# Optimization experiments

Measured on AMD Instinct MI355X. Metric: run time of the kernel, lower is better.

The kernel has to match this reference:

```python
import jax, jax.numpy as jnp
import numpy as np
import math

H = 8
C = 512
HIDE = 2048
LN_EPS = 1e-6


def setup_inputs() -> dict:
    key = jax.random.key(0)
    ks = jax.random.split(key, 9)
    B, N = 4, 2048
    std = 0.02
    return {
        "q": jax.random.normal(ks[0], (B, N, C), jnp.float32),
        "k": jax.random.normal(ks[1], (B, N, C), jnp.float32),
        "v": jax.random.normal(ks[2], (B, N, C), jnp.float32),
        "fc1_w": jax.random.normal(ks[3], (HIDE, C), jnp.float32) * std,
        "fc1_b": jnp.zeros((HIDE,), jnp.float32),
        "fc2_w": jax.random.normal(ks[4], (C, HIDE), jnp.float32) * std,
        "fc2_b": jnp.zeros((C,), jnp.float32),
        "ln1_w": jnp.ones((C,), jnp.float32),
        "ln1_b": jnp.zeros((C,), jnp.float32),
        "ln2_w": jnp.ones((C,), jnp.float32),
        "ln2_b": jnp.zeros((C,), jnp.float32),
    }


def _layernorm(x, w, b):
    mu = jnp.mean(x, axis=-1, keepdims=True)
    var = jnp.var(x, axis=-1, keepdims=True)
    return (x - mu) * jax.lax.rsqrt(var + LN_EPS) * w + b


def _mha(q, k, v):
    B, N, _ = q.shape
    hd = C // H
    # [B, H, N, hd]
    qh = q.reshape(B, N, H, hd).transpose(0, 2, 1, 3)
    kh = k.reshape(B, N, H, hd).transpose(0, 2, 1, 3)
    vh = v.reshape(B, N, H, hd).transpose(0, 2, 1, 3)
    scores = jnp.einsum('bhqd,bhkd->bhqk', qh, kh) / math.sqrt(hd)
    probs = jax.nn.softmax(scores, axis=-1)
    out = jnp.einsum('bhqk,bhkd->bhqd', probs, vh)
    return out.transpose(0, 2, 1, 3).reshape(B, N, C)


def reference(q, k, v, fc1_w, fc1_b, fc2_w, fc2_b, ln1_w, ln1_b, ln2_w, ln2_b):
    attn = _mha(q, k, v)
    q2 = _layernorm(q + attn, ln1_w, ln1_b)
    h = jax.nn.gelu(q2 @ fc1_w.T + fc1_b, approximate=False)
    mlp = h @ fc2_w.T + fc2_b
    return _layernorm(q2 + mlp, ln2_w, ln2_b)
```

## Files before the change

kernel.cpp:

```cpp
#include <hip/hip_runtime.h>
#include <math.h>

typedef unsigned short u16;
typedef __bf16 bf16_t;
typedef bf16_t bf16x4 __attribute__((ext_vector_type(4)));
typedef bf16_t bf16x8 __attribute__((ext_vector_type(8)));
typedef short s16x4 __attribute__((ext_vector_type(4)));
typedef float f32x4 __attribute__((ext_vector_type(4)));

typedef const __attribute__((address_space(1))) void* gcp;
typedef __attribute__((address_space(3))) void* lcp;

#define BB 4
#define NN 2048
#define CC 512
#define HH 8
#define HD 64
#define HIDE_ 2048
#define TT (BB*NN)

#if __has_builtin(__builtin_amdgcn_exp2f)
#define EXP2(x) __builtin_amdgcn_exp2f(x)
#else
#define EXP2(x) __expf((x) * 0.69314718055994531f)
#endif

#if __has_builtin(__builtin_amdgcn_rcpf)
#define RCP(x) __builtin_amdgcn_rcpf(x)
#else
#define RCP(x) (1.0f / (x))
#endif

__device__ __forceinline__ u16 f2bf(float f) {
  unsigned u = __float_as_uint(f);
  u += 0x7FFF + ((u >> 16) & 1);
  return (u16)(u >> 16);
}

__device__ __forceinline__ void bf8_to_f(const u16* p, float* f) {
  uint4 u = *(const uint4*)p;
  f[0] = __uint_as_float(u.x << 16); f[1] = __uint_as_float(u.x & 0xffff0000u);
  f[2] = __uint_as_float(u.y << 16); f[3] = __uint_as_float(u.y & 0xffff0000u);
  f[4] = __uint_as_float(u.z << 16); f[5] = __uint_as_float(u.z & 0xffff0000u);
  f[6] = __uint_as_float(u.w << 16); f[7] = __uint_as_float(u.w & 0xffff0000u);
}

__device__ __forceinline__ float gelu_tanh(float x) {
  float y = 0.7978845608028654f * x * (1.0f + 0.044715f * x * x);
  float a = y * 2.8853900817779268f;
  a = fminf(fmaxf(a, -30.0f), 30.0f);
  float e = EXP2(a);
  float t = (e - 1.0f) * RCP(e + 1.0f);
  return 0.5f * x * (1.0f + t);
}

__global__ __launch_bounds__(256) void prep_kernel(const float* __restrict__ q,
                                                   const float* __restrict__ k,
                                                   const float* __restrict__ fc1w,
                                                   const float* __restrict__ fc2w,
                                                   const float* __restrict__ v,
                                                   u16* __restrict__ qb,
                                                   u16* __restrict__ kb,
                                                   u16* __restrict__ w1b,
                                                   u16* __restrict__ w2b,
                                                   u16* __restrict__ vtb,
                                                   float qscale) {
  __shared__ __align__(16) u16 T[64 * 72];
  int bid = blockIdx.x, tid = threadIdx.x;
  if (bid < 5120) {
    const float* in;
    u16* out;
    int rel;
    float sc = 1.0f;
    if (bid < 2048)      { in = q;    out = qb;  rel = bid;        sc = qscale; }
    else if (bid < 4096) { in = k;    out = kb;  rel = bid - 2048; }
    else if (bid < 4608) { in = fc1w; out = w1b; rel = bid - 4096; }
    else                 { in = fc2w; out = w2b; rel = bid - 4608; }
    int i = (rel * 256 + tid) * 8;
    float4 a = *(const float4*)(in + i);
    float4 b2 = *(const float4*)(in + i + 4);
    u16 r[8] = {f2bf(a.x * sc), f2bf(a.y * sc), f2bf(a.z * sc), f2bf(a.w * sc),
                f2bf(b2.x * sc), f2bf(b2.y * sc), f2bf(b2.z * sc), f2bf(b2.w * sc)};
    *(uint4*)(out + i) = *(const uint4*)r;
    return;
  }
  int tv = bid - 5120;
  int j0 = (tv & 31) * 64;
  int bh = tv >> 5;
  int b = bh >> 3, h = bh & 7;
#pragma unroll
  for (int i = 0; i < 16; i++) {
    int idx = i * 256 + tid;
    int j = idx >> 6, d = idx & 63;
    T[d * 72 + j] = f2bf(v[((size_t)(b * NN + j0 + j)) * CC + h * 64 + d]);
  }
  __syncthreads();
#pragma unroll
  for (int i = 0; i < 16; i++) {
    int idx = i * 256 + tid;
    int d = idx >> 6, j = idx & 63;
    vtb[((size_t)(bh * 64 + d)) * NN + j0 + j] = T[d * 72 + j];
  }
}

__global__ __launch_bounds__(256, 4) void attn_kernel(const u16* __restrict__ qb,
                                                      const u16* __restrict__ kb,
                                                      const u16* __restrict__ vtb,
                                                      u16* __restrict__ ou,
                                                      float* __restrict__ lsum) {
  __shared__ __align__(16) u16 Ks[64 * 64];
  __shared__ __align__(16) u16 Vs[64 * 64];
  int tid = threadIdx.x, wave = tid >> 6, lane = tid & 63;
  int l15 = lane & 15, quad = lane >> 4;
  int r7 = l15 & 7;
  int bid = blockIdx.x;
  int half = blockIdx.y;
  int qt = bid & 15, h = (bid >> 4) & 7, b = bid >> 7;
  int qw = qt * 128 + wave * 32;
  int j0base = half * 1024;

  u16* ou_ = ou + (size_t)half * TT * CC;
  float* ls_ = lsum + (size_t)half * TT * HH;

  size_t qbase = ((size_t)(b * NN + qw + l15)) * CC + h * 64 + quad * 8;
  bf16x8 qfA0 = *(const bf16x8*)&qb[qbase];
  bf16x8 qfA1 = *(const bf16x8*)&qb[qbase + 32];
  bf16x8 qfB0 = *(const bf16x8*)&qb[qbase + (size_t)16 * CC];
  bf16x8 qfB1 = *(const bf16x8*)&qb[qbase + (size_t)16 * CC + 32];

  int rl = lane >> 3;
  int cb = (lane & 7) ^ rl;
  int rK = wave * 16 + rl;
  size_t vtbase = ((size_t)(b * HH + h)) * 64 * NN;
  const u16* kp0 = kb + ((size_t)(b * NN + j0base + rK)) * CC + h * 64 + cb * 8;
  const u16* kp1 = kp0 + (size_t)8 * CC;
  const u16* vp0 = vtb + vtbase + (size_t)rK * NN + j0base + cb * 8;
  const u16* vp1 = vp0 + (size_t)8 * NN;
  lcp lK0 = (lcp)&Ks[wave * 16 * 64];
  lcp lK1 = (lcp)&Ks[wave * 16 * 64 + 8 * 64];
  lcp lV0 = (lcp)&Vs[wave * 16 * 64];
  lcp lV1 = (lcp)&Vs[wave * 16 * 64 + 8 * 64];

  float lA = 0.f, lB = 0.f;
  f32x4 oA[4] = {}, oB[4] = {};

  for (int kt = 0; kt < 16; kt++) {
    __syncthreads();
    __builtin_amdgcn_global_load_lds((gcp)kp0, lK0, 16, 0, 0);
    __builtin_amdgcn_global_load_lds((gcp)kp1, lK1, 16, 0, 0);
    __builtin_amdgcn_global_load_lds((gcp)vp0, lV0, 16, 0, 0);
    __builtin_amdgcn_global_load_lds((gcp)vp1, lV1, 16, 0, 0);
    kp0 += (size_t)64 * CC; kp1 += (size_t)64 * CC;
    vp0 += 64; vp1 += 64;
    __syncthreads();

    s16x4 pfA[4], pfB[4];
#pragma unroll
    for (int nt = 0; nt < 4; nt++) {
      const u16* krow = &Ks[(nt * 16 + l15) * 64];
      bf16x8 k0 = *(const bf16x8*)&krow[(quad ^ r7) * 8];
      bf16x8 k1 = *(const bf16x8*)&krow[((quad + 4) ^ r7) * 8];
      f32x4 zA = {0.f, 0.f, 0.f, 0.f}, zB = {0.f, 0.f, 0.f, 0.f};
      zA = __builtin_amdgcn_mfma_f32_16x16x32_bf16(k0, qfA0, zA, 0, 0, 0);
      zA = __builtin_amdgcn_mfma_f32_16x16x32_bf16(k1, qfA1, zA, 0, 0, 0);
      zB = __builtin_amdgcn_mfma_f32_16x16x32_bf16(k0, qfB0, zB, 0, 0, 0);
      zB = __builtin_amdgcn_mfma_f32_16x16x32_bf16(k1, qfB1, zB, 0, 0, 0);
      float a0 = EXP2(zA[0]), a1 = EXP2(zA[1]), a2 = EXP2(zA[2]), a3 = EXP2(zA[3]);
      float b0 = EXP2(zB[0]), b1 = EXP2(zB[1]), b2 = EXP2(zB[2]), b3 = EXP2(zB[3]);
      lA += (a0 + a1) + (a2 + a3);
      lB += (b0 + b1) + (b2 + b3);
      bf16x4 ta = {(bf16_t)a0, (bf16_t)a1, (bf16_t)a2, (bf16_t)a3};
      bf16x4 tb = {(bf16_t)b0, (bf16_t)b1, (bf16_t)b2, (bf16_t)b3};
      pfA[nt] = __builtin_bit_cast(s16x4, ta);
      pfB[nt] = __builtin_bit_cast(s16x4, tb);
    }
#pragma unroll
    for (int dt = 0; dt < 4; dt++) {
      const u16* vrow = &Vs[(dt * 16 + l15) * 64];
#pragma unroll
      for (int nt = 0; nt < 4; nt++) {
        s16x4 vf = *(const s16x4*)
            &vrow[((nt * 2 + (quad >> 1)) ^ r7) * 8 + (quad & 1) * 4];
        oA[dt] = __builtin_amdgcn_mfma_f32_16x16x16bf16_1k(vf, pfA[nt], oA[dt], 0, 0, 0);
        oB[dt] = __builtin_amdgcn_mfma_f32_16x16x16bf16_1k(vf, pfB[nt], oB[dt], 0, 0, 0);
      }
    }
  }

  lA += __shfl_xor(lA, 16, 64);
  lA += __shfl_xor(lA, 32, 64);
  lB += __shfl_xor(lB, 16, 64);
  lB += __shfl_xor(lB, 32, 64);
  if (quad == 0) {
    ls_[(size_t)(b * NN + qw + l15) * HH + h] = lA;
    ls_[(size_t)(b * NN + qw + 16 + l15) * HH + h] = lB;
  }
  size_t obase = ((size_t)(b * NN + qw + l15)) * CC + h * 64 + quad * 4;
#pragma unroll
  for (int dt = 0; dt < 4; dt++) {
    u16 ra[4] = {f2bf(oA[dt][0]), f2bf(oA[dt][1]), f2bf(oA[dt][2]), f2bf(oA[dt][3])};
    u16 rb[4] = {f2bf(oB[dt][0]), f2bf(oB[dt][1]), f2bf(oB[dt][2]), f2bf(oB[dt][3])};
    *(uint2*)&ou_[obase + dt * 16] = *(const uint2*)ra;
    *(uint2*)&ou_[obase + (size_t)16 * CC + dt * 16] = *(const uint2*)rb;
  }
}

__global__ __launch_bounds__(256) void ln1_kernel(const u16* __restrict__ qb,
                                                  const u16* __restrict__ ou,
                                                  const float* __restrict__ lsum,
                                                  const float* __restrict__ w,
                                                  const float* __restrict__ bb,
                                                  u16* __restrict__ outb,
                                                  float inv_qs) {
  int tid = threadIdx.x;
  int row = blockIdx.x * 4 + (tid >> 6);
  int lane = tid & 63;
  int h = lane >> 3;
  size_t base = (size_t)row * CC + lane * 8;
  const u16* ou1 = ou + (size_t)TT * CC;
  const float* ls1 = lsum + (size_t)TT * HH;
  float li = lsum[(size_t)row * HH + h] + ls1[(size_t)row * HH + h];
  float inv = 1.0f / li;
  float a[8], c[8], d[8];
  bf8_to_f(qb + base, a);
  bf8_to_f(ou + base, c);
  bf8_to_f(ou1 + base, d);
  float x[8];
#pragma unroll
  for (int i = 0; i < 8; i++) x[i] = a[i] * inv_qs + (c[i] + d[i]) * inv;
  float sum = 0.f, sq = 0.f;
#pragma unroll
  for (int i = 0; i < 8; i++) { sum += x[i]; sq += x[i] * x[i]; }
#pragma unroll
  for (int msk = 1; msk < 64; msk <<= 1) {
    sum += __shfl_xor(sum, msk, 64);
    sq += __shfl_xor(sq, msk, 64);
  }
  float mu = sum * (1.0f / CC);
  float var = sq * (1.0f / CC) - mu * mu;
  float rs = rsqrtf(var + 1e-6f);
  int col = lane * 8;
  float4 w0 = *(const float4*)(w + col);
  float4 w1 = *(const float4*)(w + col + 4);
  float4 b0 = *(const float4*)(bb + col);
  float4 b1 = *(const float4*)(bb + col + 4);
  float wv[8] = {w0.x, w0.y, w0.z, w0.w, w1.x, w1.y, w1.z, w1.w};
  float bv[8] = {b0.x, b0.y, b0.z, b0.w, b1.x, b1.y, b1.z, b1.w};
  u16 r[8];
#pragma unroll
  for (int i = 0; i < 8; i++) r[i] = f2bf((x[i] - mu) * rs * wv[i] + bv[i]);
  *(uint4*)(outb + base) = *(const uint4*)r;
}

__global__ __launch_bounds__(256) void ln2_kernel(const u16* __restrict__ q2b,
                                                  const u16* __restrict__ mp,
                                                  const float* __restrict__ fb,
                                                  const float* __restrict__ w,
                                                  const float* __restrict__ bb,
                                                  float* __restrict__ outf) {
  int tid = threadIdx.x;
  int row = blockIdx.x * 4 + (tid >> 6);
  int lane = tid & 63;
  size_t base = (size_t)row * CC + lane * 8;
  const u16* mp1 = mp + (size_t)TT * CC;
  int col = lane * 8;
  float a[8], c[8], d[8];
  bf8_to_f(q2b + base, a);
  bf8_to_f(mp + base, c);
  bf8_to_f(mp1 + base, d);
  float4 f0 = *(const float4*)(fb + col);
  float4 f1 = *(const float4*)(fb + col + 4);
  float fbv[8] = {f0.x, f0.y, f0.z, f0.w, f1.x, f1.y, f1.z, f1.w};
  float x[8];
#pragma unroll
  for (int i = 0; i < 8; i++) x[i] = a[i] + c[i] + d[i] + fbv[i];
  float sum = 0.f, sq = 0.f;
#pragma unroll
  for (int i = 0; i < 8; i++) { sum += x[i]; sq += x[i] * x[i]; }
#pragma unroll
  for (int msk = 1; msk < 64; msk <<= 1) {
    sum += __shfl_xor(sum, msk, 64);
    sq += __shfl_xor(sq, msk, 64);
  }
  float mu = sum * (1.0f / CC);
  float var = sq * (1.0f / CC) - mu * mu;
  float rs = rsqrtf(var + 1e-6f);
  float4 w0 = *(const float4*)(w + col);
  float4 w1 = *(const float4*)(w + col + 4);
  float4 b0 = *(const float4*)(bb + col);
  float4 b1 = *(const float4*)(bb + col + 4);
  float wv[8] = {w0.x, w0.y, w0.z, w0.w, w1.x, w1.y, w1.z, w1.w};
  float bv[8] = {b0.x, b0.y, b0.z, b0.w, b1.x, b1.y, b1.z, b1.w};
  float y[8];
#pragma unroll
  for (int i = 0; i < 8; i++) y[i] = (x[i] - mu) * rs * wv[i] + bv[i];
  *(float4*)(outf + base) = make_float4(y[0], y[1], y[2], y[3]);
  *(float4*)(outf + base + 4) = make_float4(y[4], y[5], y[6], y[7]);
}

__global__ __launch_bounds__(256) void gemm_fc1(const u16* __restrict__ A,
                                                const u16* __restrict__ Bw,
                                                const float* __restrict__ bias,
                                                u16* __restrict__ outb,
                                                int M, int Nn, int K) {
  __shared__ __align__(16) u16 As[128 * 32];
  __shared__ __align__(16) u16 Bs[128 * 32];
  int tid = threadIdx.x, wave = tid >> 6, lane = tid & 63;
  int l15 = lane & 15, quad = lane >> 4;
  int m0 = blockIdx.y * 128, n0 = blockIdx.x * 128;
  int wm = (wave >> 1) * 64, wn = (wave & 1) * 64;
  int w32 = wave * 32;
  int lrow = lane >> 2, lcol = (lane & 3) * 8;
  const u16* Ap = &A[(size_t)(m0 + w32 + lrow) * K + lcol];
  const u16* Bp = &Bw[(size_t)(n0 + w32 + lrow) * K + lcol];
  const u16* Ap2 = Ap + (size_t)16 * K;
  const u16* Bp2 = Bp + (size_t)16 * K;
  lcp lAs0 = (lcp)&As[w32 * 32];
  lcp lAs1 = (lcp)&As[(w32 + 16) * 32];
  lcp lBs0 = (lcp)&Bs[w32 * 32];
  lcp lBs1 = (lcp)&Bs[(w32 + 16) * 32];
  f32x4 acc[4][4] = {};

  for (int kk = 0; kk < K; kk += 32) {
    __syncthreads();
    __builtin_amdgcn_global_load_lds((gcp)(Ap + kk), lAs0, 16, 0, 0);
    __builtin_amdgcn_global_load_lds((gcp)(Ap2 + kk), lAs1, 16, 0, 0);
    __builtin_amdgcn_global_load_lds((gcp)(Bp + kk), lBs0, 16, 0, 0);
    __builtin_amdgcn_global_load_lds((gcp)(Bp2 + kk), lBs1, 16, 0, 0);
    __syncthreads();
    bf16x8 af[4], bf[4];
#pragma unroll
    for (int am = 0; am < 4; am++)
      af[am] = *(const bf16x8*)&As[(wm + am * 16 + l15) * 32 + quad * 8];
#pragma unroll
    for (int bn = 0; bn < 4; bn++)
      bf[bn] = *(const bf16x8*)&Bs[(wn + bn * 16 + l15) * 32 + quad * 8];
#pragma unroll
    for (int am = 0; am < 4; am++)
#pragma unroll
      for (int bn = 0; bn < 4; bn++)
        acc[am][bn] =
            __builtin_amdgcn_mfma_f32_16x16x32_bf16(af[am], bf[bn], acc[am][bn], 0, 0, 0);
  }

#pragma unroll
  for (int am = 0; am < 4; am++)
#pragma unroll
    for (int bn = 0; bn < 4; bn++) {
      int rowi = m0 + wm + am * 16 + quad * 4;
      int col = n0 + wn + bn * 16 + l15;
      float bcol = bias[col];
#pragma unroll
      for (int r = 0; r < 4; r++) {
        float val = gelu_tanh(acc[am][bn][r] + bcol);
        outb[(size_t)(rowi + r) * Nn + col] = f2bf(val);
      }
    }
}

__global__ __launch_bounds__(256) void gemm_fc2_sk(const u16* __restrict__ A,
                                                   const u16* __restrict__ Bw,
                                                   u16* __restrict__ outb,
                                                   int M, int Nn, int K, int Ksplit) {
  __shared__ __align__(16) u16 As[128 * 32];
  __shared__ __align__(16) u16 Bs[128 * 32];
  int tid = threadIdx.x, wave = tid >> 6, lane = tid & 63;
  int l15 = lane & 15, quad = lane >> 4;
  int m0 = blockIdx.y * 128, n0 = blockIdx.x * 128;
  int kbeg = blockIdx.z * Ksplit;
  u16* outz = outb + (size_t)blockIdx.z * TT * CC;
  int wm = (wave >> 1) * 64, wn = (wave & 1) * 64;
  int w32 = wave * 32;
  int lrow = lane >> 2, lcol = (lane & 3) * 8;
  const u16* Ap = &A[(size_t)(m0 + w32 + lrow) * K + lcol];
  const u16* Bp = &Bw[(size_t)(n0 + w32 + lrow) * K + lcol];
  const u16* Ap2 = Ap + (size_t)16 * K;
  const u16* Bp2 = Bp + (size_t)16 * K;
  lcp lAs0 = (lcp)&As[w32 * 32];
  lcp lAs1 = (lcp)&As[(w32 + 16) * 32];
  lcp lBs0 = (lcp)&Bs[w32 * 32];
  lcp lBs1 = (lcp)&Bs[(w32 + 16) * 32];
  f32x4 acc[4][4] = {};

  for (int kk = kbeg; kk < kbeg + Ksplit; kk += 32) {
    __syncthreads();
    __builtin_amdgcn_global_load_lds((gcp)(Ap + kk), lAs0, 16, 0, 0);
    __builtin_amdgcn_global_load_lds((gcp)(Ap2 + kk), lAs1, 16, 0, 0);
    __builtin_amdgcn_global_load_lds((gcp)(Bp + kk), lBs0, 16, 0, 0);
    __builtin_amdgcn_global_load_lds((gcp)(Bp2 + kk), lBs1, 16, 0, 0);
    __syncthreads();
    bf16x8 af[4], bf[4];
#pragma unroll
    for (int am = 0; am < 4; am++)
      af[am] = *(const bf16x8*)&As[(wm + am * 16 + l15) * 32 + quad * 8];
#pragma unroll
    for (int bn = 0; bn < 4; bn++)
      bf[bn] = *(const bf16x8*)&Bs[(wn + bn * 16 + l15) * 32 + quad * 8];
#pragma unroll
    for (int am = 0; am < 4; am++)
#pragma unroll
      for (int bn = 0; bn < 4; bn++)
        acc[am][bn] =
            __builtin_amdgcn_mfma_f32_16x16x32_bf16(af[am], bf[bn], acc[am][bn], 0, 0, 0);
  }

#pragma unroll
  for (int am = 0; am < 4; am++)
#pragma unroll
    for (int bn = 0; bn < 4; bn++) {
      int rowi = m0 + wm + am * 16 + quad * 4;
      int col = n0 + wn + bn * 16 + l15;
#pragma unroll
      for (int r = 0; r < 4; r++)
        outz[(size_t)(rowi + r) * Nn + col] = f2bf(acc[am][bn][r]);
    }
}

extern "C" void kernel_launch(void* const* d_in, const int* in_sizes, int n_in,
                              void* d_out, int out_size, void* d_ws, size_t ws_size,
                              hipStream_t stream) {
  const float* q = (const float*)d_in[0];
  const float* k = (const float*)d_in[1];
  const float* v = (const float*)d_in[2];
  const float* fc1_w = (const float*)d_in[3];
  const float* fc1_b = (const float*)d_in[4];
  const float* fc2_w = (const float*)d_in[5];
  const float* fc2_b = (const float*)d_in[6];
  const float* ln1_w = (const float*)d_in[7];
  const float* ln1_b = (const float*)d_in[8];
  const float* ln2_w = (const float*)d_in[9];
  const float* ln2_b = (const float*)d_in[10];
  float* out = (float*)d_out;

  char* ws = (char*)d_ws;
  size_t off = 0;
  u16* qb = (u16*)(ws + off); off += (size_t)TT * CC * 2;
  u16* kb = (u16*)(ws + off); off += (size_t)TT * CC * 2;
  u16* vtb = (u16*)(ws + off); off += (size_t)TT * CC * 2;
  u16* w1b = (u16*)(ws + off); off += (size_t)HIDE_ * CC * 2;
  u16* w2b = (u16*)(ws + off); off += (size_t)CC * HIDE_ * 2;
  u16* ou = (u16*)(ws + off); off += (size_t)2 * TT * CC * 2;
  float* lsum = (float*)(ws + off); off += (size_t)2 * TT * HH * 4;
  u16* q2b = (u16*)(ws + off); off += (size_t)TT * CC * 2;
  u16* hbuf = (u16*)(ws + off); off += (size_t)TT * HIDE_ * 2;
  u16* mp = (u16*)(ws + off); off += (size_t)2 * TT * CC * 2;

  const float QS = 0.18033688011112042f;
  const float INV_QS = 5.5451774444795623f;
  prep_kernel<<<6144, 256, 0, stream>>>(q, k, fc1_w, fc2_w, v, qb, kb, w1b, w2b, vtb, QS);
  attn_kernel<<<dim3(512, 2), 256, 0, stream>>>(qb, kb, vtb, ou, lsum);
  ln1_kernel<<<2048, 256, 0, stream>>>(qb, ou, lsum, ln1_w, ln1_b, q2b, INV_QS);
  gemm_fc1<<<dim3(16, 64), 256, 0, stream>>>(q2b, w1b, fc1_b, hbuf, TT, HIDE_, CC);
  gemm_fc2_sk<<<dim3(4, 64, 2), 256, 0, stream>>>(hbuf, w2b, mp, TT, CC, HIDE_, 1024);
  ln2_kernel<<<2048, 256, 0, stream>>>(q2b, mp, fc2_b, ln2_w, ln2_b, out);
}
```

Measured before the change: 242.3 us.

## Drop bf16 q copy and deepen GEMM K-tiles to 64 with swizzled LDS

```diff
diff --git a/kernel.cpp b/kernel.cpp
--- a/kernel.cpp
+++ b/kernel.cpp
@@ -45,6 +45,14 @@
   f[6] = __uint_as_float(u.w << 16); f[7] = __uint_as_float(u.w & 0xffff0000u);
 }
 
+__device__ __forceinline__ bf16x8 ldq8(const float* p, float s) {
+  float4 a = *(const float4*)p;
+  float4 b = *(const float4*)(p + 4);
+  bf16x8 r = {(bf16_t)(a.x * s), (bf16_t)(a.y * s), (bf16_t)(a.z * s), (bf16_t)(a.w * s),
+              (bf16_t)(b.x * s), (bf16_t)(b.y * s), (bf16_t)(b.z * s), (bf16_t)(b.w * s)};
+  return r;
+}
+
 __device__ __forceinline__ float gelu_tanh(float x) {
   float y = 0.7978845608028654f * x * (1.0f + 0.044715f * x * x);
   float a = y * 2.8853900817779268f;
@@ -54,37 +62,32 @@
   return 0.5f * x * (1.0f + t);
 }
 
-__global__ __launch_bounds__(256) void prep_kernel(const float* __restrict__ q,
-                                                   const float* __restrict__ k,
+__global__ __launch_bounds__(256) void prep_kernel(const float* __restrict__ k,
                                                    const float* __restrict__ fc1w,
                                                    const float* __restrict__ fc2w,
                                                    const float* __restrict__ v,
-                                                   u16* __restrict__ qb,
                                                    u16* __restrict__ kb,
                                                    u16* __restrict__ w1b,
                                                    u16* __restrict__ w2b,
-                                                   u16* __restrict__ vtb,
-                                                   float qscale) {
+                                                   u16* __restrict__ vtb) {
   __shared__ __align__(16) u16 T[64 * 72];
   int bid = blockIdx.x, tid = threadIdx.x;
-  if (bid < 5120) {
+  if (bid < 3072) {
     const float* in;
     u16* out;
     int rel;
-    float sc = 1.0f;
-    if (bid < 2048)      { in = q;    out = qb;  rel = bid;        sc = qscale; }
-    else if (bid < 4096) { in = k;    out = kb;  rel = bid - 2048; }
-    else if (bid < 4608) { in = fc1w; out = w1b; rel = bid - 4096; }
-    else                 { in = fc2w; out = w2b; rel = bid - 4608; }
+    if (bid < 2048)      { in = k;    out = kb;  rel = bid; }
+    else if (bid < 2560) { in = fc1w; out = w1b; rel = bid - 2048; }
+    else                 { in = fc2w; out = w2b; rel = bid - 2560; }
     int i = (rel * 256 + tid) * 8;
     float4 a = *(const float4*)(in + i);
     float4 b2 = *(const float4*)(in + i + 4);
-    u16 r[8] = {f2bf(a.x * sc), f2bf(a.y * sc), f2bf(a.z * sc), f2bf(a.w * sc),
-                f2bf(b2.x * sc), f2bf(b2.y * sc), f2bf(b2.z * sc), f2bf(b2.w * sc)};
+    u16 r[8] = {f2bf(a.x), f2bf(a.y), f2bf(a.z), f2bf(a.w),
+                f2bf(b2.x), f2bf(b2.y), f2bf(b2.z), f2bf(b2.w)};
     *(uint4*)(out + i) = *(const uint4*)r;
     return;
   }
-  int tv = bid - 5120;
+  int tv = bid - 3072;
   int j0 = (tv & 31) * 64;
   int bh = tv >> 5;
   int b = bh >> 3, h = bh & 7;
@@ -103,11 +106,12 @@
   }
 }
 
-__global__ __launch_bounds__(256, 4) void attn_kernel(const u16* __restrict__ qb,
+__global__ __launch_bounds__(256, 4) void attn_kernel(const float* __restrict__ qf,
                                                       const u16* __restrict__ kb,
                                                       const u16* __restrict__ vtb,
                                                       u16* __restrict__ ou,
-                                                      float* __restrict__ lsum) {
+                                                      float* __restrict__ lsum,
+                                                      float qs) {
   __shared__ __align__(16) u16 Ks[64 * 64];
   __shared__ __align__(16) u16 Vs[64 * 64];
   int tid = threadIdx.x, wave = tid >> 6, lane = tid & 63;
@@ -122,11 +126,11 @@
   u16* ou_ = ou + (size_t)half * TT * CC;
   float* ls_ = lsum + (size_t)half * TT * HH;
 
-  size_t qbase = ((size_t)(b * NN + qw + l15)) * CC + h * 64 + quad * 8;
-  bf16x8 qfA0 = *(const bf16x8*)&qb[qbase];
-  bf16x8 qfA1 = *(const bf16x8*)&qb[qbase + 32];
-  bf16x8 qfB0 = *(const bf16x8*)&qb[qbase + (size_t)16 * CC];
-  bf16x8 qfB1 = *(const bf16x8*)&qb[qbase + (size_t)16 * CC + 32];
+  const float* qp = qf + ((size_t)(b * NN + qw + l15)) * CC + h * 64 + quad * 8;
+  bf16x8 qfA0 = ldq8(qp, qs);
+  bf16x8 qfA1 = ldq8(qp + 32, qs);
+  bf16x8 qfB0 = ldq8(qp + (size_t)16 * CC, qs);
+  bf16x8 qfB1 = ldq8(qp + (size_t)16 * CC + 32, qs);
 
   int rl = lane >> 3;
   int cb = (lane & 7) ^ rl;
@@ -205,13 +209,12 @@
   }
 }
 
-__global__ __launch_bounds__(256) void ln1_kernel(const u16* __restrict__ qb,
+__global__ __launch_bounds__(256) void ln1_kernel(const float* __restrict__ q,
                                                   const u16* __restrict__ ou,
                                                   const float* __restrict__ lsum,
                                                   const float* __restrict__ w,
                                                   const float* __restrict__ bb,
-                                                  u16* __restrict__ outb,
-                                                  float inv_qs) {
+                                                  u16* __restrict__ outb) {
   int tid = threadIdx.x;
   int row = blockIdx.x * 4 + (tid >> 6);
   int lane = tid & 63;
@@ -221,13 +224,15 @@
   const float* ls1 = lsum + (size_t)TT * HH;
   float li = lsum[(size_t)row * HH + h] + ls1[(size_t)row * HH + h];
   float inv = 1.0f / li;
-  float a[8], c[8], d[8];
-  bf8_to_f(qb + base, a);
+  float4 a0 = *(const float4*)(q + base);
+  float4 a1 = *(const float4*)(q + base + 4);
+  float c[8], d[8];
   bf8_to_f(ou + base, c);
   bf8_to_f(ou1 + base, d);
+  float av[8] = {a0.x, a0.y, a0.z, a0.w, a1.x, a1.y, a1.z, a1.w};
   float x[8];
 #pragma unroll
-  for (int i = 0; i < 8; i++) x[i] = a[i] * inv_qs + (c[i] + d[i]) * inv;
+  for (int i = 0; i < 8; i++) x[i] = av[i] + (c[i] + d[i]) * inv;
   float sum = 0.f, sq = 0.f;
 #pragma unroll
   for (int i = 0; i < 8; i++) { sum += x[i]; sq += x[i] * x[i]; }
@@ -298,49 +303,58 @@
   *(float4*)(outf + base + 4) = make_float4(y[4], y[5], y[6], y[7]);
 }
 
-__global__ __launch_bounds__(256) void gemm_fc1(const u16* __restrict__ A,
-                                                const u16* __restrict__ Bw,
-                                                const float* __restrict__ bias,
-                                                u16* __restrict__ outb,
-                                                int M, int Nn, int K) {
-  __shared__ __align__(16) u16 As[128 * 32];
-  __shared__ __align__(16) u16 Bs[128 * 32];
+template <bool GELU>
+__global__ __launch_bounds__(256) void gemm_bk64(const u16* __restrict__ A,
+                                                 const u16* __restrict__ Bw,
+                                                 const float* __restrict__ bias,
+                                                 u16* __restrict__ outb,
+                                                 int M, int Nn, int K,
+                                                 int kbeg, int kend) {
+  __shared__ __align__(16) u16 As[128 * 64];
+  __shared__ __align__(16) u16 Bs[128 * 64];
   int tid = threadIdx.x, wave = tid >> 6, lane = tid & 63;
   int l15 = lane & 15, quad = lane >> 4;
+  int r7 = l15 & 7;
   int m0 = blockIdx.y * 128, n0 = blockIdx.x * 128;
   int wm = (wave >> 1) * 64, wn = (wave & 1) * 64;
   int w32 = wave * 32;
-  int lrow = lane >> 2, lcol = (lane & 3) * 8;
-  const u16* Ap = &A[(size_t)(m0 + w32 + lrow) * K + lcol];
-  const u16* Bp = &Bw[(size_t)(n0 + w32 + lrow) * K + lcol];
-  const u16* Ap2 = Ap + (size_t)16 * K;
-  const u16* Bp2 = Bp + (size_t)16 * K;
-  lcp lAs0 = (lcp)&As[w32 * 32];
-  lcp lAs1 = (lcp)&As[(w32 + 16) * 32];
-  lcp lBs0 = (lcp)&Bs[w32 * 32];
-  lcp lBs1 = (lcp)&Bs[(w32 + 16) * 32];
+  int rl = lane >> 3;
+  int scb = (lane & 7) ^ rl;
+  const u16* Ap = &A[(size_t)(m0 + w32 + rl) * K + kbeg + scb * 8];
+  const u16* Bp = &Bw[(size_t)(n0 + w32 + rl) * K + kbeg + scb * 8];
+  lcp lAs = (lcp)&As[w32 * 64];
+  lcp lBs = (lcp)&Bs[w32 * 64];
   f32x4 acc[4][4] = {};
 
-  for (int kk = 0; kk < K; kk += 32) {
-    __syncthreads();
-    __builtin_amdgcn_global_load_lds((gcp)(Ap + kk), lAs0, 16, 0, 0);
-    __builtin_amdgcn_global_load_lds((gcp)(Ap2 + kk), lAs1, 16, 0, 0);
-    __builtin_amdgcn_global_load_lds((gcp)(Bp + kk), lBs0, 16, 0, 0);
-    __builtin_amdgcn_global_load_lds((gcp)(Bp2 + kk), lBs1, 16, 0, 0);
-    __syncthreads();
-    bf16x8 af[4], bf[4];
-#pragma unroll
-    for (int am = 0; am < 4; am++)
-      af[am] = *(const bf16x8*)&As[(wm + am * 16 + l15) * 32 + quad * 8];
-#pragma unroll
-    for (int bn = 0; bn < 4; bn++)
-      bf[bn] = *(const bf16x8*)&Bs[(wn + bn * 16 + l15) * 32 + quad * 8];
-#pragma unroll
-    for (int am = 0; am < 4; am++)
+  for (int kk = kbeg; kk < kend; kk += 64) {
+    __syncthreads();
+#pragma unroll
+    for (int c = 0; c < 4; c++) {
+      __builtin_amdgcn_global_load_lds((gcp)(Ap + (size_t)(c * 8) * K), 
+          (lcp)((__attribute__((address_space(3))) char*)lAs + c * 1024), 16, 0, 0);
+      __builtin_amdgcn_global_load_lds((gcp)(Bp + (size_t)(c * 8) * K),
+          (lcp)((__attribute__((address_space(3))) char*)lBs + c * 1024), 16, 0, 0);
+    }
+    Ap += 64; Bp += 64;
+    __syncthreads();
+#pragma unroll
+    for (int kh = 0; kh < 2; kh++) {
+      bf16x8 af[4], bf[4];
+#pragma unroll
+      for (int am = 0; am < 4; am++)
+        af[am] = *(const bf16x8*)&As[(wm + am * 16 + l15) * 64 +
+                                     (((kh * 4 + quad)) ^ r7) * 8];
 #pragma unroll
       for (int bn = 0; bn < 4; bn++)
-        acc[am][bn] =
-            __builtin_amdgcn_mfma_f32_16x16x32_bf16(af[am], bf[bn], acc[am][bn], 0, 0, 0);
+        bf[bn] = *(const bf16x8*)&Bs[(wn + bn * 16 + l15) * 64 +
+                                     (((kh * 4 + quad)) ^ r7) * 8];
+#pragma unroll
+      for (int am = 0; am < 4; am++)
+#pragma unroll
+        for (int bn = 0; bn < 4; bn++)
+          acc[am][bn] =
+              __builtin_amdgcn_mfma_f32_16x16x32_bf16(af[am], bf[bn], acc[am][bn], 0, 0, 0);
+    }
   }
 
 #pragma unroll
@@ -349,10 +363,11 @@
     for (int bn = 0; bn < 4; bn++) {
       int rowi = m0 + wm + am * 16 + quad * 4;
       int col = n0 + wn + bn * 16 + l15;
-      float bcol = bias[col];
+      float bcol = GELU ? bias[col] : 0.0f;
 #pragma unroll
       for (int r = 0; r < 4; r++) {
-        float val = gelu_tanh(acc[am][bn][r] + bcol);
+        float val = acc[am][bn][r] + bcol;
+        if (GELU) val = gelu_tanh(val);
         outb[(size_t)(rowi + r) * Nn + col] = f2bf(val);
       }
     }
@@ -362,46 +377,53 @@
                                                    const u16* __restrict__ Bw,
                                                    u16* __restrict__ outb,
                                                    int M, int Nn, int K, int Ksplit) {
-  __shared__ __align__(16) u16 As[128 * 32];
-  __shared__ __align__(16) u16 Bs[128 * 32];
+  __shared__ __align__(16) u16 As[128 * 64];
+  __shared__ __align__(16) u16 Bs[128 * 64];
   int tid = threadIdx.x, wave = tid >> 6, lane = tid & 63;
   int l15 = lane & 15, quad = lane >> 4;
+  int r7 = l15 & 7;
   int m0 = blockIdx.y * 128, n0 = blockIdx.x * 128;
-  int kbeg = blockIdx.z * Ksplit;
+  int kbeg = blockIdx.z * Ksplit, kend = kbeg + Ksplit;
   u16* outz = outb + (size_t)blockIdx.z * TT * CC;
   int wm = (wave >> 1) * 64, wn = (wave & 1) * 64;
   int w32 = wave * 32;
-  int lrow = lane >> 2, lcol = (lane & 3) * 8;
-  const u16* Ap = &A[(size_t)(m0 + w32 + lrow) * K + lcol];
-  const u16* Bp = &Bw[(size_t)(n0 + w32 + lrow) * K + lcol];
-  const u16* Ap2 = Ap + (size_t)16 * K;
-  const u16* Bp2 = Bp + (size_t)16 * K;
-  lcp lAs0 = (lcp)&As[w32 * 32];
-  lcp lAs1 = (lcp)&As[(w32 + 16) * 32];
-  lcp lBs0 = (lcp)&Bs[w32 * 32];
-  lcp lBs1 = (lcp)&Bs[(w32 + 16) * 32];
+  int rl = lane >> 3;
+  int scb = (lane & 7) ^ rl;
+  const u16* Ap = &A[(size_t)(m0 + w32 + rl) * K + kbeg + scb * 8];
+  const u16* Bp = &Bw[(size_t)(n0 + w32 + rl) * K + kbeg + scb * 8];
+  lcp lAs = (lcp)&As[w32 * 64];
+  lcp lBs = (lcp)&Bs[w32 * 64];
   f32x4 acc[4][4] = {};
 
-  for (int kk = kbeg; kk < kbeg + Ksplit; kk += 32) {
-    __syncthreads();
-    __builtin_amdgcn_global_load_lds((gcp)(Ap + kk), lAs0, 16, 0, 0);
-    __builtin_amdgcn_global_load_lds((gcp)(Ap2 + kk), lAs1, 16, 0, 0);
-    __builtin_amdgcn_global_load_lds((gcp)(Bp + kk), lBs0, 16, 0, 0);
-    __builtin_amdgcn_global_load_lds((gcp)(Bp2 + kk), lBs1, 16, 0, 0);
-    __syncthreads();
-    bf16x8 af[4], bf[4];
-#pragma unroll
-    for (int am = 0; am < 4; am++)
-      af[am] = *(const bf16x8*)&As[(wm + am * 16 + l15) * 32 + quad * 8];
-#pragma unroll
-    for (int bn = 0; bn < 4; bn++)
-      bf[bn] = *(const bf16x8*)&Bs[(wn + bn * 16 + l15) * 32 + quad * 8];
-#pragma unroll
-    for (int am = 0; am < 4; am++)
+  for (int kk = kbeg; kk < kend; kk += 64) {
+    __syncthreads();
+#pragma unroll
+    for (int c = 0; c < 4; c++) {
+      __builtin_amdgcn_global_load_lds((gcp)(Ap + (size_t)(c * 8) * K),
+          (lcp)((__attribute__((address_space(3))) char*)lAs + c * 1024), 16, 0, 0);
+      __builtin_amdgcn_global_load_lds((gcp)(Bp + (size_t)(c * 8) * K),
+          (lcp)((__attribute__((address_space(3))) char*)lBs + c * 1024), 16, 0, 0);
+    }
+    Ap += 64; Bp += 64;
+    __syncthreads();
+#pragma unroll
+    for (int kh = 0; kh < 2; kh++) {
+      bf16x8 af[4], bf[4];
+#pragma unroll
+      for (int am = 0; am < 4; am++)
+        af[am] = *(const bf16x8*)&As[(wm + am * 16 + l15) * 64 +
+                                     (((kh * 4 + quad)) ^ r7) * 8];
 #pragma unroll
       for (int bn = 0; bn < 4; bn++)
-        acc[am][bn] =
-            __builtin_amdgcn_mfma_f32_16x16x32_bf16(af[am], bf[bn], acc[am][bn], 0, 0, 0);
+        bf[bn] = *(const bf16x8*)&Bs[(wn + bn * 16 + l15) * 64 +
+                                     (((kh * 4 + quad)) ^ r7) * 8];
+#pragma unroll
+      for (int am = 0; am < 4; am++)
+#pragma unroll
+        for (int bn = 0; bn < 4; bn++)
+          acc[am][bn] =
+              __builtin_amdgcn_mfma_f32_16x16x32_bf16(af[am], bf[bn], acc[am][bn], 0, 0, 0);
+    }
   }
 
 #pragma unroll
@@ -434,7 +456,6 @@
 
   char* ws = (char*)d_ws;
   size_t off = 0;
-  u16* qb = (u16*)(ws + off); off += (size_t)TT * CC * 2;
   u16* kb = (u16*)(ws + off); off += (size_t)TT * CC * 2;
   u16* vtb = (u16*)(ws + off); off += (size_t)TT * CC * 2;
   u16* w1b = (u16*)(ws + off); off += (size_t)HIDE_ * CC * 2;
@@ -446,11 +467,11 @@
   u16* mp = (u16*)(ws + off); off += (size_t)2 * TT * CC * 2;
 
   const float QS = 0.18033688011112042f;
-  const float INV_QS = 5.5451774444795623f;
-  prep_kernel<<<6144, 256, 0, stream>>>(q, k, fc1_w, fc2_w, v, qb, kb, w1b, w2b, vtb, QS);
-  attn_kernel<<<dim3(512, 2), 256, 0, stream>>>(qb, kb, vtb, ou, lsum);
-  ln1_kernel<<<2048, 256, 0, stream>>>(qb, ou, lsum, ln1_w, ln1_b, q2b, INV_QS);
-  gemm_fc1<<<dim3(16, 64), 256, 0, stream>>>(q2b, w1b, fc1_b, hbuf, TT, HIDE_, CC);
+  prep_kernel<<<4096, 256, 0, stream>>>(k, fc1_w, fc2_w, v, kb, w1b, w2b, vtb);
+  attn_kernel<<<dim3(512, 2), 256, 0, stream>>>(q, kb, vtb, ou, lsum, QS);
+  ln1_kernel<<<2048, 256, 0, stream>>>(q, ou, lsum, ln1_w, ln1_b, q2b);
+  gemm_bk64<true><<<dim3(16, 64), 256, 0, stream>>>(q2b, w1b, fc1_b, hbuf,
+                                                    TT, HIDE_, CC, 0, CC);
   gemm_fc2_sk<<<dim3(4, 64, 2), 256, 0, stream>>>(hbuf, w2b, mp, TT, CC, HIDE_, 1024);
   ln2_kernel<<<2048, 256, 0, stream>>>(q2b, mp, fc2_b, ln2_w, ln2_b, out);
 }
```

After: 226.2 us. 6.7% less time.
